# Performance work log

Measured on AMD Instinct MI355X. Metric: run time of the kernel, lower is better.

Reference implementation:

```python
import jax, jax.numpy as jnp
import numpy as np

H, DM, N, K, R = 768, 1536, 16, 4, 48  # hidden, intermediate, state, conv kernel, dt rank
B, L = 2, 1024


def _silu(x):
    return x * jax.nn.sigmoid(x)


def _causal_conv(x, w, b):
    # x: [B, D, L]; w: [D, K] depthwise; causal left-pad K-1 (matches causal_conv1d_fn)
    out = jax.lax.conv_general_dilated(
        x, w[:, None, :], window_strides=(1,), padding=[(K - 1, 0)],
        feature_group_count=w.shape[0], dimension_numbers=('NCH', 'OIH', 'NCH'))
    return out + b[None, :, None]


def _selective_scan(u, delta, A, Bm, Cm, Dp, gate):
    # u/delta/gate: [B, D, L]; A: [D, N]; Bm/Cm: [B, L, N]; Dp: [D]
    dA = jnp.exp(delta[:, :, :, None] * A[None, :, None, :])              # [B,D,L,N]
    dBu = delta[:, :, :, None] * Bm[:, None, :, :] * u[:, :, :, None]      # [B,D,L,N]
    dA_t = jnp.moveaxis(dA, 2, 0)    # [L,B,D,N]
    dBu_t = jnp.moveaxis(dBu, 2, 0)  # [L,B,D,N]
    C_t = jnp.moveaxis(Cm, 1, 0)     # [L,B,N]

    def step(x, inp):
        a, bu, c = inp
        x = a * x + bu                               # [B,D,N]
        y = jnp.einsum('bdn,bn->bd', x, c)
        return x, y

    x0 = jnp.zeros(dA_t.shape[1:], dA_t.dtype)
    _, ys = jax.lax.scan(step, x0, (dA_t, dBu_t, C_t))
    y = jnp.moveaxis(ys, 0, 2) + u * Dp[None, :, None]   # [B,D,L]
    return y * _silu(gate)


def _branch(conv_out, gate, xw, dtw, dtb, Alog, Dp):
    # conv_out/gate: [B, D, L]
    ssm = jnp.einsum('bdl,pd->blp', conv_out, xw)        # [B,L,R+2N]
    ts, Bm, Cm = ssm[..., :R], ssm[..., R:R + N], ssm[..., R + N:]
    delta = jax.nn.softplus(jnp.einsum('dr,blr->bdl', dtw, ts) + dtb[None, :, None])
    A = -jnp.exp(Alog)
    return _selective_scan(conv_out, delta, A, Bm, Cm, Dp, gate)


def setup_inputs() -> dict:
    key = jax.random.key(0)
    ks = jax.random.split(key, 12)
    s = 0.02
    hidden_states = jax.random.normal(ks[0], (B, L, H), jnp.float32)
    in_proj_w = jax.random.normal(ks[1], (2 * DM, H), jnp.float32) * s
    conv_w = jax.random.normal(ks[2], (DM, K), jnp.float32) * 0.3
    conv_b = jax.random.normal(ks[3], (DM,), jnp.float32) * s
    x_proj_w = jax.random.normal(ks[4], (R + 2 * N, DM), jnp.float32) * s
    dt_proj_w = jax.random.normal(ks[5], (DM, R), jnp.float32) * s
    dt_proj_b = -4.0 + 0.1 * jax.random.normal(ks[6], (DM,), jnp.float32)
    x_proj_back_w = jax.random.normal(ks[7], (R + 2 * N, DM), jnp.float32) * s
    dt_proj_back_w = jax.random.normal(ks[8], (DM, R), jnp.float32) * s
    dt_proj_back_b = -4.0 + 0.1 * jax.random.normal(ks[9], (DM,), jnp.float32)
    A_log = jnp.log(jnp.broadcast_to(jnp.arange(1, N + 1, dtype=jnp.float32)[None, :], (DM, N)))
    A_log_back = A_log
    D = jnp.ones((DM,), jnp.float32)
    D_back = jnp.ones((DM,), jnp.float32)
    out_proj_w = jax.random.normal(ks[10], (H, DM), jnp.float32) * s
    return {
        'hidden_states': hidden_states, 'in_proj_w': in_proj_w,
        'conv_w': conv_w, 'conv_b': conv_b,
        'x_proj_w': x_proj_w, 'dt_proj_w': dt_proj_w, 'dt_proj_b': dt_proj_b,
        'x_proj_back_w': x_proj_back_w, 'dt_proj_back_w': dt_proj_back_w,
        'dt_proj_back_b': dt_proj_back_b, 'A_log': A_log, 'A_log_back': A_log_back,
        'D': D, 'D_back': D_back, 'out_proj_w': out_proj_w,
    }


def reference(hidden_states, in_proj_w, conv_w, conv_b, x_proj_w, dt_proj_w,
              dt_proj_b, x_proj_back_w, dt_proj_back_w, dt_proj_back_b,
              A_log, A_log_back, D, D_back, out_proj_w):
    proj = jnp.einsum('blh,ph->bpl', hidden_states, in_proj_w)  # [B,2D,L]
    x, gate = proj[:, :DM], proj[:, DM:]
    conv_out = _silu(_causal_conv(x, conv_w, conv_b))           # [B,D,L]
    # forward-direction scan
    y_f = _branch(conv_out, gate, x_proj_w, dt_proj_w, dt_proj_b, A_log, D)
    # backward-direction scan on time-flipped conv output and gate
    y_b = _branch(conv_out[:, :, ::-1], gate[:, :, ::-1], x_proj_back_w,
                  dt_proj_back_w, dt_proj_back_b, A_log_back, D_back)
    y = y_f + y_b[:, :, ::-1]
    return jnp.einsum('bdl,hd->blh', y, out_proj_w)
```

## Files before the change

### kernel.cpp

```cpp
#include <hip/hip_runtime.h>
#include <math.h>

constexpr int cH  = 768;
constexpr int cDM = 1536;
constexpr int cN  = 16;
constexpr int cR  = 48;
constexpr int cB  = 2;
constexpr int cL  = 1024;
constexpr int cPS = 160;
constexpr int cCK = 32;

typedef unsigned short u16;
typedef __attribute__((ext_vector_type(8))) short bf16x8;
typedef __attribute__((ext_vector_type(4))) float f32x4;

__device__ __forceinline__ u16 f2bf(float f) {
    unsigned u = __float_as_uint(f);
    u += 0x7FFF + ((u >> 16) & 1);
    return (u16)(u >> 16);
}
__device__ __forceinline__ float bf2f(u16 h) {
    return __uint_as_float((unsigned)h << 16);
}

__global__ __launch_bounds__(256)
void prep_kernel(const float* __restrict__ hid, const float* __restrict__ inw,
                 const float* __restrict__ xpw, const float* __restrict__ xpbw,
                 const float* __restrict__ outw, const float* __restrict__ dtw,
                 const float* __restrict__ dtbw,
                 u16* __restrict__ hid_b, u16* __restrict__ inw_b,
                 u16* __restrict__ xpw2_b, u16* __restrict__ outw_b,
                 u16* __restrict__ dtw2_b)
{
    const long i8 = ((long)blockIdx.x * 256 + threadIdx.x) * 8;
    const long e0 = 1572864;
    const long e1 = e0 + 2359296;
    const long e2 = e1 + 122880;
    const long e3 = e2 + 122880;
    const long e4 = e3 + 1179648;
    const long e5 = e4 + 98304;
    const long e6 = e5 + 98304;
    const float* in; u16* out; long off; int pad = 0;
    if      (i8 < e0) { in = hid;  out = hid_b;           off = i8; }
    else if (i8 < e1) { in = inw;  out = inw_b;           off = i8 - e0; }
    else if (i8 < e2) { in = xpw;  out = xpw2_b;          off = i8 - e1; }
    else if (i8 < e3) { in = xpbw; out = xpw2_b + 122880; off = i8 - e2; }
    else if (i8 < e4) { in = outw; out = outw_b;          off = i8 - e3; }
    else if (i8 < e5) { in = dtw;  out = dtw2_b;          off = i8 - e4; pad = 1; }
    else if (i8 < e6) { in = dtbw; out = dtw2_b + 98304;  off = i8 - e5; pad = 1; }
    else return;
    u16 o[8];
    if (!pad) {
        const float4 a = *(const float4*)&in[off];
        const float4 b = *(const float4*)&in[off + 4];
        o[0]=f2bf(a.x); o[1]=f2bf(a.y); o[2]=f2bf(a.z); o[3]=f2bf(a.w);
        o[4]=f2bf(b.x); o[5]=f2bf(b.y); o[6]=f2bf(b.z); o[7]=f2bf(b.w);
    } else {
        const long r = off >> 6; const int k0 = (int)(off & 63);
        #pragma unroll
        for (int k = 0; k < 8; ++k)
            o[k] = (k0 + k < cR) ? f2bf(in[r * cR + k0 + k]) : (u16)0;
    }
    *(uint4*)&out[off] = *(uint4*)o;
}

__global__ __launch_bounds__(256)
void tspad_kernel(const float* __restrict__ ssms, u16* __restrict__ out) {
    int i = blockIdx.x * 256 + threadIdx.x;
    int dirsel = i >> 17;
    int rem = i & 131071;
    int bl = rem >> 6, k = rem & 63;
    out[i] = (k < cR) ? f2bf(ssms[(long)bl * cPS + dirsel * 80 + k]) : (u16)0;
}

__global__ __launch_bounds__(256)
void comb_kernel(u16* __restrict__ yf, const u16* __restrict__ yb, long n8) {
    long i = (long)blockIdx.x * 256 + threadIdx.x;
    if (i >= n8) return;
    uint4 av = ((uint4*)yf)[i];
    uint4 bv = ((const uint4*)yb)[i];
    unsigned* ap = (unsigned*)&av;
    unsigned* bp = (unsigned*)&bv;
    #pragma unroll
    for (int j = 0; j < 4; ++j) {
        const float lo = bf2f((u16)(ap[j] & 0xffff)) + bf2f((u16)(bp[j] & 0xffff));
        const float hi = bf2f((u16)(ap[j] >> 16))    + bf2f((u16)(bp[j] >> 16));
        ap[j] = (unsigned)f2bf(lo) | ((unsigned)f2bf(hi) << 16);
    }
    ((uint4*)yf)[i] = av;
}

__device__ __forceinline__ void gld_lds16(const u16* g, u16* l) {
    __builtin_amdgcn_global_load_lds(
        (const __attribute__((address_space(1))) unsigned int*)g,
        (__attribute__((address_space(3))) unsigned int*)l, 16, 0, 0);
}

#define GST(SA, SB, k0) do {                                                   \
    _Pragma("unroll")                                                          \
    for (int h = 0; h < 3; ++h) {                                              \
        const int q  = wid * 3 + h;                                            \
        const int rw = lane >> 2;                                              \
        if (q < 4) {                                                           \
            const int r  = q * 16 + rw;                                        \
            const int sw = (r & 3) ^ ((r >> 2) & 3);                           \
            const int kg = (k0) + (((lane & 3) ^ sw) << 3);                    \
            gld_lds16(Ab + (long)(m0 + r) * lda + kg, &SA[q * 512]);           \
        } else {                                                               \
            const int r  = (q - 4) * 16 + rw;                                  \
            const int sw = (r & 3) ^ ((r >> 2) & 3);                           \
            const int kg = (k0) + (((lane & 3) ^ sw) << 3);                    \
            int nr = n0 + r; if (nr > N2 - 1) nr = N2 - 1;                     \
            gld_lds16(Bb + (long)nr * ldb + kg, &SB[(q - 4) * 512]);           \
        }                                                                      \
    }                                                                          \
} while (0)

#define CMP(SA, SB) do {                                                       \
    bf16x8 af[4], bfr[2];                                                      \
    _Pragma("unroll")                                                          \
    for (int i = 0; i < 4; ++i) {                                              \
        const int ra  = i * 16 + lr;                                           \
        const int swa = (ra & 3) ^ ((ra >> 2) & 3);                            \
        af[i] = *(const bf16x8*)&SA[ra * 32 + ((lc ^ swa) << 3)];              \
    }                                                                          \
    _Pragma("unroll")                                                          \
    for (int j = 0; j < 2; ++j) {                                              \
        const int rb  = wn + j * 16 + lr;                                      \
        const int swb = (rb & 3) ^ ((rb >> 2) & 3);                            \
        bfr[j] = *(const bf16x8*)&SB[rb * 32 + ((lc ^ swb) << 3)];             \
    }                                                                          \
    _Pragma("unroll")                                                          \
    for (int i = 0; i < 4; ++i)                                                \
        _Pragma("unroll")                                                      \
        for (int j = 0; j < 2; ++j)                                            \
            acc[i][j] = __builtin_amdgcn_mfma_f32_16x16x32_bf16(af[i], bfr[j], acc[i][j], 0, 0, 0); \
} while (0)

template<int EPI>
__global__ __launch_bounds__(256, 4)
void gemm_mfma(const u16* __restrict__ A, const u16* __restrict__ B,
               float* __restrict__ C0, float* __restrict__ C1,
               const float* __restrict__ bias,
               int N2, int Kd, int lda, int ldb, int ldc,
               long sA, long sC, int splitCol, int kspl)
{
    __shared__ __align__(16) u16 shA0[2048];
    __shared__ __align__(16) u16 shA1[2048];
    __shared__ __align__(16) u16 shB0[4096];
    __shared__ __align__(16) u16 shB1[4096];
    const int tid  = threadIdx.x;
    const int wid  = tid >> 6, lane = tid & 63;
    const int lr   = lane & 15, lc = lane >> 4;
    const int z    = blockIdx.z;
    const int bz   = z / kspl, ks = z % kspl;
    const int kpc  = Kd / kspl;
    const int kbeg = ks * kpc;
    const int nt   = kpc / 32;
    const int n0 = blockIdx.x * 128, m0 = blockIdx.y * 64;
    const int wn = wid * 32;

    const u16* Ab = A + (long)bz * sA;
    const u16* Bb = B;

    f32x4 acc[4][2] = {};

    GST(shA0, shB0, kbeg);
    __syncthreads();
    int t = 0;
    for (;;) {
        if (t + 1 < nt) GST(shA1, shB1, kbeg + (t + 1) * 32);
        CMP(shA0, shB0);
        __syncthreads();
        if (++t >= nt) break;
        if (t + 1 < nt) GST(shA0, shB0, kbeg + (t + 1) * 32);
        CMP(shA1, shB1);
        __syncthreads();
        if (++t >= nt) break;
    }

    #pragma unroll
    for (int i = 0; i < 4; ++i) {
        #pragma unroll
        for (int e = 0; e < 4; ++e) {
            const int m = m0 + i * 16 + lc * 4 + e;
            float* base0 = C0 + (long)bz * sC + (long)m * ldc;
            float* base1 = (C1 != nullptr) ? C1 + (long)bz * sC + (long)m * ldc : nullptr;
            #pragma unroll
            for (int j = 0; j < 2; ++j) {
                const int n = n0 + wn + j * 16 + lr;
                if (n < N2) {
                    float v = acc[i][j][e];
                    if (EPI == 1) {
                        const float t2 = v + bias[n];
                        v = fmaxf(t2, 0.f) + __logf(1.f + __expf(-fabsf(t2)));
                    }
                    float* cp = (base1 && n >= splitCol) ? base1 + (n - splitCol)
                                                         : base0 + n;
                    if (EPI == 2) atomicAdd(cp, v);
                    else          *cp = v;
                }
            }
        }
    }
}

__global__ __launch_bounds__(256)
void conv_silu2(const float* __restrict__ x, const float* __restrict__ cw,
                const float* __restrict__ cb,
                float* __restrict__ convTf, u16* __restrict__ convT_b)
{
    __shared__ float xt[35][64];
    const int l0 = blockIdx.x * 32, d0 = blockIdx.y * 64, b = blockIdx.z;
    const int tid = threadIdx.x;
    for (int i = tid; i < 35 * 64; i += 256) {
        const int r = i >> 6, c = i & 63;
        const int l = l0 - 3 + r;
        xt[r][c] = (l >= 0) ? x[((long)b * cL + l) * cDM + d0 + c] : 0.f;
    }
    __syncthreads();
    const int dc = tid & 63, lsub = tid >> 6;
    const int d = d0 + dc;
    const float w0 = cw[d*4], w1 = cw[d*4+1], w2 = cw[d*4+2], w3 = cw[d*4+3];
    const float bi = cb[d];
    #pragma unroll
    for (int k = 0; k < 8; ++k) {
        const int row = lsub * 8 + k;
        float v = bi;
        v = fmaf(w0, xt[row][dc],     v);
        v = fmaf(w1, xt[row + 1][dc], v);
        v = fmaf(w2, xt[row + 2][dc], v);
        v = fmaf(w3, xt[row + 3][dc], v);
        const float s = v / (1.f + __expf(-v));
        const long o = ((long)b * cL + l0 + row) * cDM + d;
        convTf[o] = s;
        convT_b[o] = f2bf(s);
    }
}

#define SA_LOAD(g, DU, UU) _Pragma("unroll")                                   \
    for (int k = 0; k < 4; ++k) {                                              \
        const int t_ = (g) * 4 + k;                                            \
        const int l_ = dir ? (base - t_) : (base + t_);                        \
        DU[k] = dT[(long)l_ * cDM + d]; UU[k] = uT[(long)l_ * cDM + d];        \
    }

#define SA_COMP(g, DU, UU) _Pragma("unroll")                                   \
    for (int k = 0; k < 4; ++k) {                                              \
        const int t_ = (g) * 4 + k;                                            \
        const float du_ = DU[k]; const float duu_ = du_ * UU[k];               \
        const float4 b0_ = *(const float4*)&bcA[t_][half * 8];                 \
        const float4 b1_ = *(const float4*)&bcA[t_][half * 8 + 4];             \
        const float bb_[8] = {b0_.x,b0_.y,b0_.z,b0_.w,b1_.x,b1_.y,b1_.z,b1_.w};\
        _Pragma("unroll")                                                      \
        for (int n = 0; n < 8; ++n) {                                          \
            const float dA_ = __expf(du_ * a[n]);                              \
            xs[n] = fmaf(dA_, xs[n], duu_ * bb_[n]);                           \
            Ap[n] *= dA_;                                                      \
        }                                                                      \
    }

__global__ __launch_bounds__(64, 2)
void scanA_kernel(const float* __restrict__ dT0, const float* __restrict__ dT1,
                  const float* __restrict__ uF, const float* __restrict__ ssms,
                  const float* __restrict__ AlogF, const float* __restrict__ AlogB,
                  float* __restrict__ Ap_out, float* __restrict__ Xf_out)
{
    __shared__ float bcA[32][16];
    const int lane = threadIdx.x;
    const int dd = lane & 31, half = lane >> 5;
    const int d = blockIdx.x * 32 + dd;
    const int b = blockIdx.y;
    const int z = blockIdx.z;
    const int dir = z >> 5, ck = z & 31;
    const float* Alog = dir ? AlogB : AlogF;
    const float* dT = (dir ? dT1 : dT0) + (long)b * cL * cDM;
    const float* uT = uF + (long)b * cL * cDM;
    const float* sp = ssms + (long)b * cL * cPS;
    const int sofs = dir ? 128 : 48;
    const int base = dir ? (cL - 1 - ck * 32) : (ck * 32);

    #pragma unroll
    for (int h = 0; h < 2; ++h) {
        const int idx = h * 64 + lane;
        const int r = idx >> 2, q = idx & 3;
        const int lr_ = dir ? (base - r) : (base + r);
        *(float4*)&bcA[r][q * 4] = *(const float4*)&sp[(long)lr_ * cPS + sofs + q * 4];
    }
    float a[8];
    {
        const float4 a0 = *(const float4*)&Alog[d * 16 + half * 8];
        const float4 a1 = *(const float4*)&Alog[d * 16 + half * 8 + 4];
        a[0]=-__expf(a0.x); a[1]=-__expf(a0.y); a[2]=-__expf(a0.z); a[3]=-__expf(a0.w);
        a[4]=-__expf(a1.x); a[5]=-__expf(a1.y); a[6]=-__expf(a1.z); a[7]=-__expf(a1.w);
    }
    __syncthreads();

    float xs[8] = {};
    float Ap[8];
    #pragma unroll
    for (int n = 0; n < 8; ++n) Ap[n] = 1.f;

    float duA[4], uuA[4], duB[4], uuB[4];
    SA_LOAD(0, duA, uuA);
    SA_LOAD(1, duB, uuB);
    SA_COMP(0, duA, uuA);
    SA_LOAD(2, duA, uuA);
    SA_COMP(1, duB, uuB);
    SA_LOAD(3, duB, uuB);
    SA_COMP(2, duA, uuA);
    SA_LOAD(4, duA, uuA);
    SA_COMP(3, duB, uuB);
    SA_LOAD(5, duB, uuB);
    SA_COMP(4, duA, uuA);
    SA_LOAD(6, duA, uuA);
    SA_COMP(5, duB, uuB);
    SA_LOAD(7, duB, uuB);
    SA_COMP(6, duA, uuA);
    SA_COMP(7, duB, uuB);

    const long ob = (((long)(b * 2 + dir) * cCK + ck) * cDM + d) * 16 + half * 8;
    *(float4*)&Ap_out[ob]     = make_float4(Ap[0], Ap[1], Ap[2], Ap[3]);
    *(float4*)&Ap_out[ob + 4] = make_float4(Ap[4], Ap[5], Ap[6], Ap[7]);
    *(float4*)&Xf_out[ob]     = make_float4(xs[0], xs[1], xs[2], xs[3]);
    *(float4*)&Xf_out[ob + 4] = make_float4(xs[4], xs[5], xs[6], xs[7]);
}

__global__ __launch_bounds__(256)
void scanB_kernel(float* __restrict__ Ap, const float* __restrict__ Xf)
{
    const int gid = blockIdx.x * 256 + threadIdx.x;
    const int n = gid & 15;
    const int rest = gid >> 4;
    const int d = rest % cDM;
    const int b2 = rest / cDM;
    float x0 = 0.f;
    #pragma unroll
    for (int c = 0; c < cCK; ++c) {
        const long idx = (((long)b2 * cCK + c) * cDM + d) * 16 + n;
        const float ap = Ap[idx], xf = Xf[idx];
        Ap[idx] = x0;
        x0 = fmaf(ap, x0, xf);
    }
}

#define SC_LOAD(g, DU, UU, GV) _Pragma("unroll")                               \
    for (int k = 0; k < 4; ++k) {                                              \
        const int t_ = (g) * 4 + k;                                            \
        const int l_ = dir ? (base - t_) : (base + t_);                        \
        const long off_ = (long)l_ * cDM + d;                                  \
        DU[k] = dT[off_]; UU[k] = uT[off_]; GV[k] = gT[off_];                  \
    }

#define SC_COMP(g, DU, UU, GV) _Pragma("unroll")                               \
    for (int k = 0; k < 4; ++k) {                                              \
        const int t_ = (g) * 4 + k;                                            \
        const float du_ = DU[k]; const float uu_ = UU[k];                      \
        const float duu_ = du_ * uu_;                                          \
        const float4 b0_ = *(const float4*)&bc[t_][half * 8];                  \
        const float4 b1_ = *(const float4*)&bc[t_][half * 8 + 4];              \
        const float4 c0_ = *(const float4*)&bc[t_][16 + half * 8];             \
        const float4 c1_ = *(const float4*)&bc[t_][16 + half * 8 + 4];         \
        const float bb_[8] = {b0_.x,b0_.y,b0_.z,b0_.w,b1_.x,b1_.y,b1_.z,b1_.w};\
        const float cc_[8] = {c0_.x,c0_.y,c0_.z,c0_.w,c1_.x,c1_.y,c1_.z,c1_.w};\
        float y_ = 0.f;                                                        \
        _Pragma("unroll")                                                      \
        for (int n = 0; n < 8; ++n) {                                          \
            const float dA_ = __expf(du_ * a[n]);                              \
            xs[n] = fmaf(dA_, xs[n], duu_ * bb_[n]);                           \
            y_ = fmaf(xs[n], cc_[n], y_);                                      \
        }                                                                      \
        y_ += __shfl_xor(y_, 32);                                              \
        if (half == 0) {                                                       \
            const int l2_ = dir ? (base - t_) : (base + t_);                   \
            const float gv_ = GV[k];                                           \
            const float val_ = (y_ + uu_ * Dd) * (gv_ / (1.f + __expf(-gv_))); \
            yout[((long)b * cL + l2_) * cDM + d] = f2bf(val_);                 \
        }                                                                      \
    }

__global__ __launch_bounds__(64, 2)
void scanC_kernel(const float* __restrict__ dT0, const float* __restrict__ dT1,
                  const float* __restrict__ uF, const float* __restrict__ gF,
                  const float* __restrict__ ssms,
                  const float* __restrict__ AlogF, const float* __restrict__ AlogB,
                  const float* __restrict__ Df, const float* __restrict__ Db,
                  const float* __restrict__ X0,
                  u16* __restrict__ yf, u16* __restrict__ yb)
{
    __shared__ float bc[32][32];
    const int lane = threadIdx.x;
    const int dd = lane & 31, half = lane >> 5;
    const int d = blockIdx.x * 32 + dd;
    const int b = blockIdx.y;
    const int z = blockIdx.z;
    const int dir = z >> 5, ck = z & 31;
    const float* Alog = dir ? AlogB : AlogF;
    const float* dT = (dir ? dT1 : dT0) + (long)b * cL * cDM;
    const float* uT = uF + (long)b * cL * cDM;
    const float* gT = gF + (long)b * cL * cDM;
    const float* sp = ssms + (long)b * cL * cPS;
    const float Dd = dir ? Db[d] : Df[d];
    u16* yout = dir ? yb : yf;
    const int sofs = dir ? 128 : 48;
    const int base = dir ? (cL - 1 - ck * 32) : (ck * 32);

    #pragma unroll
    for (int h = 0; h < 4; ++h) {
        const int idx = h * 64 + lane;
        const int r = idx >> 3, q = idx & 7;
        const int lr_ = dir ? (base - r) : (base + r);
        *(float4*)&bc[r][q * 4] = *(const float4*)&sp[(long)lr_ * cPS + sofs + q * 4];
    }
    float a[8];
    {
        const float4 a0 = *(const float4*)&Alog[d * 16 + half * 8];
        const float4 a1 = *(const float4*)&Alog[d * 16 + half * 8 + 4];
        a[0]=-__expf(a0.x); a[1]=-__expf(a0.y); a[2]=-__expf(a0.z); a[3]=-__expf(a0.w);
        a[4]=-__expf(a1.x); a[5]=-__expf(a1.y); a[6]=-__expf(a1.z); a[7]=-__expf(a1.w);
    }
    float xs[8];
    {
        const long ob = (((long)(b * 2 + dir) * cCK + ck) * cDM + d) * 16 + half * 8;
        const float4 x0v = *(const float4*)&X0[ob];
        const float4 x1v = *(const float4*)&X0[ob + 4];
        xs[0]=x0v.x; xs[1]=x0v.y; xs[2]=x0v.z; xs[3]=x0v.w;
        xs[4]=x1v.x; xs[5]=x1v.y; xs[6]=x1v.z; xs[7]=x1v.w;
    }
    __syncthreads();

    float duA[4], uuA[4], gvA[4], duB[4], uuB[4], gvB[4];
    SC_LOAD(0, duA, uuA, gvA);
    SC_LOAD(1, duB, uuB, gvB);
    SC_COMP(0, duA, uuA, gvA);
    SC_LOAD(2, duA, uuA, gvA);
    SC_COMP(1, duB, uuB, gvB);
    SC_LOAD(3, duB, uuB, gvB);
    SC_COMP(2, duA, uuA, gvA);
    SC_LOAD(4, duA, uuA, gvA);
    SC_COMP(3, duB, uuB, gvB);
    SC_LOAD(5, duB, uuB, gvB);
    SC_COMP(4, duA, uuA, gvA);
    SC_LOAD(6, duA, uuA, gvA);
    SC_COMP(5, duB, uuB, gvB);
    SC_LOAD(7, duB, uuB, gvB);
    SC_COMP(6, duA, uuA, gvA);
    SC_COMP(7, duB, uuB, gvB);
}

extern "C" void kernel_launch(void* const* d_in, const int* in_sizes, int n_in,
                              void* d_out, int out_size, void* d_ws, size_t ws_size,
                              hipStream_t stream)
{
    const float* hid   = (const float*)d_in[0];
    const float* inw   = (const float*)d_in[1];
    const float* convw = (const float*)d_in[2];
    const float* convb = (const float*)d_in[3];
    const float* xpw   = (const float*)d_in[4];
    const float* dtw   = (const float*)d_in[5];
    const float* dtb   = (const float*)d_in[6];
    const float* xpbw  = (const float*)d_in[7];
    const float* dtbw  = (const float*)d_in[8];
    const float* dtbb  = (const float*)d_in[9];
    const float* Alog  = (const float*)d_in[10];
    const float* Alogb = (const float*)d_in[11];
    const float* Dv    = (const float*)d_in[12];
    const float* Dbv   = (const float*)d_in[13];
    const float* outw  = (const float*)d_in[14];
    float* out = (float*)d_out;

    float* ws = (float*)d_ws;
    const long S = (long)cB * cDM * cL;
    float* xbuf   = ws;
    float* gate   = ws + S;
    float* convTf = ws + 2 * S;
    float* deltaT1= ws + 3 * S;
    float* ssms   = ws + 4 * S;
    u16* up0      = (u16*)(ssms + (long)cB * cL * cPS);
    u16* convT_b  = up0;
    u16* ts2_b    = up0 + S;
    u16* xpw2_b   = ts2_b + (long)2 * cB * cL * 64;
    u16* dtw2_b   = xpw2_b + (long)cPS * cDM;
    u16* outw_b   = dtw2_b + (long)2 * cDM * 64;
    u16* pool2    = outw_b + (long)cH * cDM;
    u16* inw_b    = pool2;
    u16* hid_b    = pool2 + (long)2 * cDM * cH;
    u16* yf_b     = convT_b;
    u16* yb_b     = pool2;
    const long nSum = (long)2 * cB * cCK * cDM * 16;
    float* sumAp  = (float*)(pool2 + 3932160);
    float* sumXf  = sumAp + nSum;

    const dim3 blk(256);

    prep_kernel<<<dim3(2713), blk, 0, stream>>>(
        hid, inw, xpw, xpbw, outw, dtw, dtbw,
        hid_b, inw_b, xpw2_b, outw_b, dtw2_b);

    hipMemsetAsync(ssms, 0, (long)cB * cL * cPS * sizeof(float), stream);
    hipMemsetAsync(out, 0, (long)out_size * sizeof(float), stream);

    gemm_mfma<0><<<dim3(24, 16, cB), blk, 0, stream>>>(
        hid_b, inw_b, xbuf, gate, nullptr,
        2 * cDM, cH, cH, cH, cDM, (long)cL * cH, (long)cL * cDM, cDM, 1);

    conv_silu2<<<dim3(32, 24, cB), blk, 0, stream>>>(
        xbuf, convw, convb, convTf, convT_b);

    gemm_mfma<2><<<dim3(2, 16, cB * 8), blk, 0, stream>>>(
        convT_b, xpw2_b, ssms, nullptr, nullptr,
        cPS, cDM, cDM, cDM, cPS, (long)cL * cDM, (long)cL * cPS, 1 << 30, 8);

    tspad_kernel<<<1024, blk, 0, stream>>>(ssms, ts2_b);

    gemm_mfma<1><<<dim3(12, 16, cB), blk, 0, stream>>>(
        ts2_b, dtw2_b, xbuf, nullptr, dtb,
        cDM, 64, 64, 64, cDM, (long)cL * 64, (long)cL * cDM, 1 << 30, 1);
    gemm_mfma<1><<<dim3(12, 16, cB), blk, 0, stream>>>(
        ts2_b + (long)2 * cL * 64, dtw2_b + (long)cDM * 64, deltaT1, nullptr, dtbb,
        cDM, 64, 64, 64, cDM, (long)cL * 64, (long)cL * cDM, 1 << 30, 1);

    scanA_kernel<<<dim3(48, cB, 2 * cCK), dim3(64), 0, stream>>>(
        xbuf, deltaT1, convTf, ssms, Alog, Alogb, sumAp, sumXf);
    scanB_kernel<<<dim3(384), blk, 0, stream>>>(sumAp, sumXf);
    scanC_kernel<<<dim3(48, cB, 2 * cCK), dim3(64), 0, stream>>>(
        xbuf, deltaT1, convTf, gate, ssms, Alog, Alogb, Dv, Dbv,
        sumAp , yf_b, yb_b);

    comb_kernel<<<(int)(S / 8 / 256), blk, 0, stream>>>(yf_b, yb_b, S / 8);

    gemm_mfma<2><<<dim3(6, 16, cB * 2), blk, 0, stream>>>(
        yf_b, outw_b, out, nullptr, nullptr,
        cH, cDM, cDM, cDM, cH, (long)cL * cDM, (long)cL * cH, 1 << 30, 2);
}
```

Baseline: 181.6 us.

## Use raw exp2 with prescaled A, closed-form chunk decay, triple-buffered scan loads

The scan kernels now fold log2(e) into A and call the hardware v_exp_f32 directly instead of __expf. scanA no longer keeps a running product of per-step decays; it sums delta over the chunk and computes the chunk decay once at the end as exp2(sum*A). Both scan kernels move from double- to triple-buffered global loads and raise launch bounds to 4 blocks per CU to hide more latency. The closed-form product can differ slightly in rounding from the step-by-step product, and the extra buffers raise register pressure against the higher occupancy target.

```diff
diff --git a/kernel.cpp b/kernel.cpp
--- a/kernel.cpp
+++ b/kernel.cpp
@@ -22,6 +22,10 @@
 __device__ __forceinline__ float bf2f(u16 h) {
     return __uint_as_float((unsigned)h << 16);
 }
+__device__ __forceinline__ float fexp2(float x) {
+    float r; asm("v_exp_f32 %0, %1" : "=v"(r) : "v"(x)); return r;
+}
+constexpr float cLOG2E = 1.44269504f;
 
 __global__ __launch_bounds__(256)
 void prep_kernel(const float* __restrict__ hid, const float* __restrict__ inw,
@@ -249,18 +253,16 @@
     for (int k = 0; k < 4; ++k) {                                              \
         const int t_ = (g) * 4 + k;                                            \
         const float du_ = DU[k]; const float duu_ = du_ * UU[k];               \
+        sdu += du_;                                                            \
         const float4 b0_ = *(const float4*)&bcA[t_][half * 8];                 \
         const float4 b1_ = *(const float4*)&bcA[t_][half * 8 + 4];             \
         const float bb_[8] = {b0_.x,b0_.y,b0_.z,b0_.w,b1_.x,b1_.y,b1_.z,b1_.w};\
         _Pragma("unroll")                                                      \
-        for (int n = 0; n < 8; ++n) {                                          \
-            const float dA_ = __expf(du_ * a[n]);                              \
-            xs[n] = fmaf(dA_, xs[n], duu_ * bb_[n]);                           \
-            Ap[n] *= dA_;                                                      \
-        }                                                                      \
-    }
-
-__global__ __launch_bounds__(64, 2)
+        for (int n = 0; n < 8; ++n)                                            \
+            xs[n] = fmaf(fexp2(du_ * a2[n]), xs[n], duu_ * bb_[n]);            \
+    }
+
+__global__ __launch_bounds__(64, 4)
 void scanA_kernel(const float* __restrict__ dT0, const float* __restrict__ dT1,
                   const float* __restrict__ uF, const float* __restrict__ ssms,
                   const float* __restrict__ AlogF, const float* __restrict__ AlogB,
@@ -287,41 +289,38 @@
         const int lr_ = dir ? (base - r) : (base + r);
         *(float4*)&bcA[r][q * 4] = *(const float4*)&sp[(long)lr_ * cPS + sofs + q * 4];
     }
-    float a[8];
+    float a2[8];
     {
         const float4 a0 = *(const float4*)&Alog[d * 16 + half * 8];
         const float4 a1 = *(const float4*)&Alog[d * 16 + half * 8 + 4];
-        a[0]=-__expf(a0.x); a[1]=-__expf(a0.y); a[2]=-__expf(a0.z); a[3]=-__expf(a0.w);
-        a[4]=-__expf(a1.x); a[5]=-__expf(a1.y); a[6]=-__expf(a1.z); a[7]=-__expf(a1.w);
+        a2[0]=-__expf(a0.x)*cLOG2E; a2[1]=-__expf(a0.y)*cLOG2E;
+        a2[2]=-__expf(a0.z)*cLOG2E; a2[3]=-__expf(a0.w)*cLOG2E;
+        a2[4]=-__expf(a1.x)*cLOG2E; a2[5]=-__expf(a1.y)*cLOG2E;
+        a2[6]=-__expf(a1.z)*cLOG2E; a2[7]=-__expf(a1.w)*cLOG2E;
     }
     __syncthreads();
 
     float xs[8] = {};
-    float Ap[8];
-    #pragma unroll
-    for (int n = 0; n < 8; ++n) Ap[n] = 1.f;
-
-    float duA[4], uuA[4], duB[4], uuB[4];
-    SA_LOAD(0, duA, uuA);
-    SA_LOAD(1, duB, uuB);
-    SA_COMP(0, duA, uuA);
-    SA_LOAD(2, duA, uuA);
-    SA_COMP(1, duB, uuB);
-    SA_LOAD(3, duB, uuB);
-    SA_COMP(2, duA, uuA);
-    SA_LOAD(4, duA, uuA);
-    SA_COMP(3, duB, uuB);
-    SA_LOAD(5, duB, uuB);
-    SA_COMP(4, duA, uuA);
-    SA_LOAD(6, duA, uuA);
-    SA_COMP(5, duB, uuB);
-    SA_LOAD(7, duB, uuB);
-    SA_COMP(6, duA, uuA);
-    SA_COMP(7, duB, uuB);
+    float sdu = 0.f;
+
+    float dX[4], uX[4], dY[4], uY[4], dZ[4], uZ[4];
+    SA_LOAD(0, dX, uX);
+    SA_LOAD(1, dY, uY);
+    SA_LOAD(2, dZ, uZ);
+    SA_COMP(0, dX, uX); SA_LOAD(3, dX, uX);
+    SA_COMP(1, dY, uY); SA_LOAD(4, dY, uY);
+    SA_COMP(2, dZ, uZ); SA_LOAD(5, dZ, uZ);
+    SA_COMP(3, dX, uX); SA_LOAD(6, dX, uX);
+    SA_COMP(4, dY, uY); SA_LOAD(7, dY, uY);
+    SA_COMP(5, dZ, uZ);
+    SA_COMP(6, dX, uX);
+    SA_COMP(7, dY, uY);
 
     const long ob = (((long)(b * 2 + dir) * cCK + ck) * cDM + d) * 16 + half * 8;
-    *(float4*)&Ap_out[ob]     = make_float4(Ap[0], Ap[1], Ap[2], Ap[3]);
-    *(float4*)&Ap_out[ob + 4] = make_float4(Ap[4], Ap[5], Ap[6], Ap[7]);
+    *(float4*)&Ap_out[ob]     = make_float4(fexp2(sdu*a2[0]), fexp2(sdu*a2[1]),
+                                            fexp2(sdu*a2[2]), fexp2(sdu*a2[3]));
+    *(float4*)&Ap_out[ob + 4] = make_float4(fexp2(sdu*a2[4]), fexp2(sdu*a2[5]),
+                                            fexp2(sdu*a2[6]), fexp2(sdu*a2[7]));
     *(float4*)&Xf_out[ob]     = make_float4(xs[0], xs[1], xs[2], xs[3]);
     *(float4*)&Xf_out[ob + 4] = make_float4(xs[4], xs[5], xs[6], xs[7]);
 }
@@ -366,8 +365,7 @@
         float y_ = 0.f;                                                        \
         _Pragma("unroll")                                                      \
         for (int n = 0; n < 8; ++n) {                                          \
-            const float dA_ = __expf(du_ * a[n]);                              \
-            xs[n] = fmaf(dA_, xs[n], duu_ * bb_[n]);                           \
+            xs[n] = fmaf(fexp2(du_ * a2[n]), xs[n], duu_ * bb_[n]);            \
             y_ = fmaf(xs[n], cc_[n], y_);                                      \
         }                                                                      \
         y_ += __shfl_xor(y_, 32);                                              \
@@ -379,7 +377,7 @@
         }                                                                      \
     }
 
-__global__ __launch_bounds__(64, 2)
+__global__ __launch_bounds__(64, 4)
 void scanC_kernel(const float* __restrict__ dT0, const float* __restrict__ dT1,
                   const float* __restrict__ uF, const float* __restrict__ gF,
                   const float* __restrict__ ssms,
@@ -412,12 +410,14 @@
         const int lr_ = dir ? (base - r) : (base + r);
         *(float4*)&bc[r][q * 4] = *(const float4*)&sp[(long)lr_ * cPS + sofs + q * 4];
     }
-    float a[8];
+    float a2[8];
     {
         const float4 a0 = *(const float4*)&Alog[d * 16 + half * 8];
         const float4 a1 = *(const float4*)&Alog[d * 16 + half * 8 + 4];
-        a[0]=-__expf(a0.x); a[1]=-__expf(a0.y); a[2]=-__expf(a0.z); a[3]=-__expf(a0.w);
-        a[4]=-__expf(a1.x); a[5]=-__expf(a1.y); a[6]=-__expf(a1.z); a[7]=-__expf(a1.w);
+        a2[0]=-__expf(a0.x)*cLOG2E; a2[1]=-__expf(a0.y)*cLOG2E;
+        a2[2]=-__expf(a0.z)*cLOG2E; a2[3]=-__expf(a0.w)*cLOG2E;
+        a2[4]=-__expf(a1.x)*cLOG2E; a2[5]=-__expf(a1.y)*cLOG2E;
+        a2[6]=-__expf(a1.z)*cLOG2E; a2[7]=-__expf(a1.w)*cLOG2E;
     }
     float xs[8];
     {
@@ -429,23 +429,18 @@
     }
     __syncthreads();
 
-    float duA[4], uuA[4], gvA[4], duB[4], uuB[4], gvB[4];
-    SC_LOAD(0, duA, uuA, gvA);
-    SC_LOAD(1, duB, uuB, gvB);
-    SC_COMP(0, duA, uuA, gvA);
-    SC_LOAD(2, duA, uuA, gvA);
-    SC_COMP(1, duB, uuB, gvB);
-    SC_LOAD(3, duB, uuB, gvB);
-    SC_COMP(2, duA, uuA, gvA);
-    SC_LOAD(4, duA, uuA, gvA);
-    SC_COMP(3, duB, uuB, gvB);
-    SC_LOAD(5, duB, uuB, gvB);
-    SC_COMP(4, duA, uuA, gvA);
-    SC_LOAD(6, duA, uuA, gvA);
-    SC_COMP(5, duB, uuB, gvB);
-    SC_LOAD(7, duB, uuB, gvB);
-    SC_COMP(6, duA, uuA, gvA);
-    SC_COMP(7, duB, uuB, gvB);
+    float dX[4], uX[4], gX[4], dY[4], uY[4], gY[4], dZ[4], uZ[4], gZ[4];
+    SC_LOAD(0, dX, uX, gX);
+    SC_LOAD(1, dY, uY, gY);
+    SC_LOAD(2, dZ, uZ, gZ);
+    SC_COMP(0, dX, uX, gX); SC_LOAD(3, dX, uX, gX);
+    SC_COMP(1, dY, uY, gY); SC_LOAD(4, dY, uY, gY);
+    SC_COMP(2, dZ, uZ, gZ); SC_LOAD(5, dZ, uZ, gZ);
+    SC_COMP(3, dX, uX, gX); SC_LOAD(6, dX, uX, gX);
+    SC_COMP(4, dY, uY, gY); SC_LOAD(7, dY, uY, gY);
+    SC_COMP(5, dZ, uZ, gZ);
+    SC_COMP(6, dX, uX, gX);
+    SC_COMP(7, dY, uY, gY);
 }
 
 extern "C" void kernel_launch(void* const* d_in, const int* in_sizes, int n_in,
```

Result: faster. 170.3 us (-6.2%).
